# Kernel tuning notes

Hardware: AMD Instinct MI355X
Metric: run time of the kernel (lower is better)

The kernel has to match this reference:

```python
import jax, jax.numpy as jnp
import numpy as np

T = 1048576      # signal length
K = 3            # number of IMFs
ALPHA = 2000.0   # bandwidth penalty
TAU = 1e-7       # dual ascent step
TOL = 1e-6       # convergence tolerance
N_ITER = 50      # max fixed-point iterations


def _vmd(x, omega_init):
    T_ = x.shape[0]
    t = jnp.arange(1, T_ + 1, dtype=jnp.float32) / T_
    freqs = t - 0.5 - 1.0 / T_                           # [T]
    f_hat = jnp.fft.fftshift(jnp.fft.fft(x))             # [T] complex
    u0 = jnp.zeros((K, T_), dtype=f_hat.dtype)
    lam0 = jnp.zeros((T_,), dtype=f_hat.dtype)

    def step(carry, n):
        u_prev, lam_prev, omega, done = carry
        base = (freqs[None, :] - omega[:, None]) ** 2    # [K,T]
        # mode k's denom also gets (freqs-omega[k-1])^2 and (freqs-omega[k+1])^2
        nbr = jnp.zeros_like(base).at[1:].add(base[:-1]).at[:-1].add(base[1:])
        denom = base + nbr + TAU ** 2
        u_hat = (f_hat[None, :] - lam_prev[None, :] / 2.0) / (1.0 + ALPHA * denom)
        pw = jnp.real(u_hat) ** 2 + jnp.imag(u_hat) ** 2  # |u_hat|^2, [K,T]
        omega_new = jnp.sum(freqs[None, :] * pw, axis=1) / jnp.sum(pw, axis=1)
        lam_new = lam_prev + TAU * (jnp.sum(u_hat, axis=0) - f_hat)
        # convergence check (every 10th iter), mirrors the original break
        u_diff = jnp.sum(jnp.abs(u_hat - u_prev) ** 2) / jnp.sum(jnp.abs(u_prev) ** 2)
        om_diff = jnp.sum(jnp.abs(omega_new - jnp.roll(omega_new, 1))) / K
        conv = (n % 10 == 0) & (u_diff < TOL) & (om_diff < TOL)
        # freeze state once converged (break-iteration's fresh u_hat is kept)
        u_out = jnp.where(done, u_prev, u_hat)
        lam_out = jnp.where(done, lam_prev, lam_new)
        om_out = jnp.where(done, omega, omega_new)
        return (u_out, lam_out, om_out, done | conv), None

    init = (u0, lam0, omega_init.astype(jnp.float32), jnp.array(False))
    (u_hat, _, _, _), _ = jax.lax.scan(jax.checkpoint(step), init, jnp.arange(N_ITER))
    imfs = jnp.real(jnp.fft.ifft(jnp.fft.ifftshift(u_hat, axes=-1), axis=-1))
    return imfs.astype(jnp.float32)                      # [K,T]


def setup_inputs() -> dict:
    key = jax.random.key(0)
    kx, ko = jax.random.split(key)
    x = jax.random.normal(kx, (T,), dtype=jnp.float32)
    omega_init = jax.random.uniform(ko, (K,), dtype=jnp.float32) * 0.5  # init==1
    return {"x": x, "omega_init": omega_init}


def reference(x, omega_init):
    return _vmd(x, omega_init)
```

## Files before the change

kernel.cpp:

```cpp
#include <hip/hip_runtime.h>
#include <math.h>


#define ALPHA_F 2000.0f
#define TAU_F   1e-7f

static __device__ __forceinline__ int lpad2(int i) { return i + (i >> 4); }
static __device__ __forceinline__ int swz(int i)  { return ((i & 7) << 7) | (i >> 3); }
static __device__ __forceinline__ int swzA(int i) { return ((i & 7) << 6) | (i >> 3); }
static __device__ __forceinline__ float frcp(float x) { return __builtin_amdgcn_rcpf(x); }

typedef float v2f __attribute__((ext_vector_type(2)));
static __device__ __forceinline__ v2f sp(float s) { v2f r; r.x = s; r.y = s; return r; }
static __device__ __forceinline__ v2f v2(float a, float b) { v2f r; r.x = a; r.y = b; return r; }
static __device__ __forceinline__ v2f pkfma(v2f a, v2f b, v2f c)
{ return __builtin_elementwise_fma(a, b, c); }
static __device__ __forceinline__ v2f cmul(v2f a, v2f w)
{
  v2f t = a * sp(w.x);
  v2f s = v2(-a.y, a.x);
  return pkfma(s, sp(w.y), t);
}
static __device__ __forceinline__ v2f cmulrr(v2f a, float wr, float wi)
{
  v2f t = a * sp(wr);
  v2f s = v2(-a.y, a.x);
  return pkfma(s, sp(wi), t);
}

#define PADN2 1088

template<int CTRL>
static __device__ __forceinline__ float dpp_addf(float v)
{
  int r = __builtin_amdgcn_update_dpp(0, __float_as_int(v), CTRL, 0xf, 0xf, true);
  return v + __int_as_float(r);
}
static __device__ __forceinline__ float wave64_sum(float v)
{
  v = dpp_addf<0x111>(v);
  v = dpp_addf<0x112>(v);
  v = dpp_addf<0x114>(v);
  v = dpp_addf<0x118>(v);
  v = dpp_addf<0x142>(v);
  v = dpp_addf<0x143>(v);
  return v;
}
static __device__ __forceinline__ float row8_sum(float v)
{
  v = dpp_addf<0x111>(v);
  v = dpp_addf<0x112>(v);
  v = dpp_addf<0x114>(v);
  return v;
}
static __device__ __forceinline__ float rdlane(float v, int l)
{
  return __int_as_float(__builtin_amdgcn_readlane(__float_as_int(v), l));
}

template<int SIGN>
static __device__ __forceinline__ void bfly4(v2f Y0, v2f Y1, v2f Y2, v2f Y3,
    float w1r, float w1i, float w2r, float w2i, float w3r, float w3i,
    v2f& o0, v2f& o1, v2f& o2, v2f& o3)
{
  v2f y1 = cmulrr(Y1, w1r, w1i), y2 = cmulrr(Y2, w2r, w2i),
      y3 = cmulrr(Y3, w3r, w3i);
  v2f t0 = Y0 + y2, t1 = Y0 - y2, t2 = y1 + y3, t3 = y1 - y3;
  o0 = t0 + t2; o2 = t0 - t2;
  v2f ns3 = v2(t3.y, -t3.x);
  if (SIGN < 0) { o1 = t1 + ns3; o3 = t1 - ns3; }
  else          { o1 = t1 - ns3; o3 = t1 + ns3; }
}
template<int SIGN>
static __device__ __forceinline__ void bfly4_nt(v2f X0, v2f X1, v2f X2, v2f X3,
    v2f& o0, v2f& o1, v2f& o2, v2f& o3)
{
  v2f t0 = X0 + X2, t1 = X0 - X2, t2 = X1 + X3, t3 = X1 - X3;
  o0 = t0 + t2; o2 = t0 - t2;
  v2f ns3 = v2(t3.y, -t3.x);
  if (SIGN < 0) { o1 = t1 + ns3; o3 = t1 - ns3; }
  else          { o1 = t1 - ns3; o3 = t1 + ns3; }
}

template<int SIGN>
static __device__ void fft1024p_reg(v2f X0, v2f X1, v2f X2, v2f X3,
                                    v2f* A, v2f* B)
{
  const int u = threadIdx.x;
  {
    v2f o0, o1, o2, o3;
    bfly4_nt<SIGN>(X0, X1, X2, X3, o0, o1, o2, o3);
    const int base = u << 2;
    B[lpad2(base    )] = o0; B[lpad2(base + 1)] = o1;
    B[lpad2(base + 2)] = o2; B[lpad2(base + 3)] = o3;
    __syncthreads();
  }
#pragma unroll
  for (int st = 1; st < 5; ++st) {
    v2f *in  = (st & 1) ? B : A;
    v2f *out = (st & 1) ? A : B;
    const int quarter = 1 << (2 * st);
    const int p = u & (quarter - 1);
    const int g = u >> (2 * st);

    float sw, cw;
    sincospif((float)(2 * p) * (1.0f / (float)(4 << (2 * st))), &sw, &cw);
    const float w1r = cw, w1i = (SIGN < 0) ? -sw : sw;
    const float w2r = w1r * w1r - w1i * w1i, w2i = 2.0f * w1r * w1i;
    const float w3r = w2r * w1r - w2i * w1i, w3i = w2r * w1i + w2i * w1r;

    v2f o0, o1, o2, o3;
    bfly4<SIGN>(in[lpad2(u)], in[lpad2(u + 256)],
                in[lpad2(u + 512)], in[lpad2(u + 768)],
                w1r, w1i, w2r, w2i, w3r, w3i, o0, o1, o2, o3);

    const int base = (g << (2 * st + 2)) + p;
    out[lpad2(base              )] = o0;
    out[lpad2(base +     quarter)] = o1;
    out[lpad2(base + 2 * quarter)] = o2;
    out[lpad2(base + 3 * quarter)] = o3;
    __syncthreads();
  }
}

template<int SIGN>
static __device__ void fft1024p_dual(const v2f X[4], const v2f Y[4],
                                     v2f* A1, v2f* B1, v2f* A2, v2f* B2)
{
  const int u = threadIdx.x;
  {
    v2f o0, o1, o2, o3, p0, p1, p2, p3;
    bfly4_nt<SIGN>(X[0], X[1], X[2], X[3], o0, o1, o2, o3);
    bfly4_nt<SIGN>(Y[0], Y[1], Y[2], Y[3], p0, p1, p2, p3);
    const int base = u << 2;
    B1[lpad2(base    )] = o0; B1[lpad2(base + 1)] = o1;
    B1[lpad2(base + 2)] = o2; B1[lpad2(base + 3)] = o3;
    B2[lpad2(base    )] = p0; B2[lpad2(base + 1)] = p1;
    B2[lpad2(base + 2)] = p2; B2[lpad2(base + 3)] = p3;
    __syncthreads();
  }
#pragma unroll
  for (int st = 1; st < 5; ++st) {
    v2f *in1  = (st & 1) ? B1 : A1, *out1 = (st & 1) ? A1 : B1;
    v2f *in2  = (st & 1) ? B2 : A2, *out2 = (st & 1) ? A2 : B2;
    const int quarter = 1 << (2 * st);
    const int p = u & (quarter - 1);
    const int g = u >> (2 * st);

    float sw, cw;
    sincospif((float)(2 * p) * (1.0f / (float)(4 << (2 * st))), &sw, &cw);
    const float w1r = cw, w1i = (SIGN < 0) ? -sw : sw;
    const float w2r = w1r * w1r - w1i * w1i, w2i = 2.0f * w1r * w1i;
    const float w3r = w2r * w1r - w2i * w1i, w3i = w2r * w1i + w2i * w1r;

    v2f o0, o1, o2, o3, p0, p1, p2, p3;
    bfly4<SIGN>(in1[lpad2(u)], in1[lpad2(u + 256)],
                in1[lpad2(u + 512)], in1[lpad2(u + 768)],
                w1r, w1i, w2r, w2i, w3r, w3i, o0, o1, o2, o3);
    bfly4<SIGN>(in2[lpad2(u)], in2[lpad2(u + 256)],
                in2[lpad2(u + 512)], in2[lpad2(u + 768)],
                w1r, w1i, w2r, w2i, w3r, w3i, p0, p1, p2, p3);

    const int base = (g << (2 * st + 2)) + p;
    out1[lpad2(base              )] = o0;
    out1[lpad2(base +     quarter)] = o1;
    out1[lpad2(base + 2 * quarter)] = o2;
    out1[lpad2(base + 3 * quarter)] = o3;
    out2[lpad2(base              )] = p0;
    out2[lpad2(base +     quarter)] = p1;
    out2[lpad2(base + 2 * quarter)] = p2;
    out2[lpad2(base + 3 * quarter)] = p3;
    __syncthreads();
  }
}

__global__ __launch_bounds__(256) void k_fwd_passA(const float* __restrict__ x,
                                                   float2* __restrict__ ws0)
{
  __shared__ __align__(16) v2f A[PADN2], B[PADN2];
  const int p = swzA(blockIdx.x);
  const int tid = threadIdx.x;
  const int c0 = 2 * p;
  v2f X[4];
#pragma unroll
  for (int q = 0; q < 4; ++q)
    X[q] = ((const v2f*)x)[(size_t)(tid + 256 * q) * 512 + p];
  fft1024p_reg<-1>(X[0], X[1], X[2], X[3], A, B);

  float sa, ca, sb, cb, ssa, cca, ssb, ccb;
  sincospif((float)(c0 * tid) * (2.0f / 1048576.0f), &sa, &ca);
  sincospif((float)((c0 + 1) * tid) * (2.0f / 1048576.0f), &sb, &cb);
  sincospif((float)c0 * (1.0f / 2048.0f), &ssa, &cca);
  sincospif((float)(c0 + 1) * (1.0f / 2048.0f), &ssb, &ccb);
  v2f E0 = v2(ca, -sa), E1 = v2(cb, -sb);
  const v2f S0 = v2(cca, -ssa), S1 = v2(ccb, -ssb);
#pragma unroll
  for (int q = 0; q < 4; ++q) {
    int k = tid + 256 * q;
    int kk = (1024 - k) & 1023;
    v2f Z = B[lpad2(k)];
    v2f Wv = B[lpad2(kk)];
    float X0r = 0.5f * (Z.x + Wv.x), X0i = 0.5f * (Z.y - Wv.y);
    float X1r = 0.5f * (Z.y + Wv.y), X1i = 0.5f * (Wv.x - Z.x);
    v2f o01 = cmul(v2(X0r, X0i), E0);
    v2f o23 = cmul(v2(X1r, X1i), E1);
    float4 o = make_float4(o01.x, o01.y, o23.x, o23.y);
    ((float4*)ws0)[(size_t)k * 512 + p] = o;
    E0 = cmul(E0, S0); E1 = cmul(E1, S1);
  }
}

__global__ __launch_bounds__(256) void k_fwd_passB(const float2* __restrict__ ws0,
                                                   float2* __restrict__ fhat,
                                                   float* __restrict__ ET)
{
  __shared__ __align__(16) v2f A[PADN2], B[PADN2];
  const int b = swz(blockIdx.x);
  const int tid = threadIdx.x;
  v2f X[4];
#pragma unroll
  for (int q = 0; q < 4; ++q)
    X[q] = ((const v2f*)ws0)[(size_t)b * 1024 + tid + 256 * q];
  fft1024p_reg<-1>(X[0], X[1], X[2], X[3], A, B);
#pragma unroll
  for (int q = 0; q < 4; ++q) {
    int k2 = tid + 256 * q;
    v2f v = B[lpad2(k2)];
    fhat[(size_t)b * 1024 + k2] = make_float2(v.x, v.y);
    ET[(size_t)k2 * 1024 + b] = v.x * v.x + v.y * v.y;
  }
}

static __device__ __forceinline__ void lag4(float x, float& l0, float& l1,
                                            float& l2, float& l3)
{
  float m0 = x, m1 = x - (1.0f / 3.0f), m2 = x - (2.0f / 3.0f), m3 = x - 1.0f;
  l0 = -4.5f * m1 * m2 * m3;
  l1 = 13.5f * m0 * m2 * m3;
  l2 = -13.5f * m0 * m1 * m3;
  l3 =  4.5f * m0 * m1 * m2;
}

__global__ __launch_bounds__(256) void k_moments(const float* __restrict__ ET,
                                                 double* __restrict__ W)
{
  __shared__ double red[4 * 4];
  const int B = blockIdx.x;
  const int k2 = B ^ 512;
  const int tid = threadIdx.x;
  double a0 = 0, a1 = 0, a2 = 0, a3 = 0;
#pragma unroll
  for (int q = 0; q < 4; ++q) {
    int k1 = tid + 256 * q;
    float e = ET[(size_t)k2 * 1024 + k1];
    float l0, l1, l2, l3;
    lag4((float)k1 * (1.0f / 1024.0f), l0, l1, l2, l3);
    a0 += (double)(e * l0); a1 += (double)(e * l1);
    a2 += (double)(e * l2); a3 += (double)(e * l3);
  }
  const int lane = tid & 63, wv = tid >> 6;
  double pv[4] = { a0, a1, a2, a3 };
#pragma unroll
  for (int j = 0; j < 4; ++j) {
    double v = pv[j];
    for (int off = 32; off; off >>= 1) v += __shfl_down(v, off, 64);
    if (lane == 0) red[wv * 4 + j] = v;
  }
  __syncthreads();
  if (tid < 4)
    W[B * 4 + tid] = red[tid] + red[4 + tid] + red[8 + tid] + red[12 + tid];
}

__global__ __launch_bounds__(512) void k_solve(
    const double* __restrict__ W4, const float* __restrict__ omega_init,
    float* __restrict__ ckeepN, float* __restrict__ omegaF)
{
  __shared__ float red[2][64];
  const int t = threadIdx.x;
  const int lane = t & 63, wv = t >> 6;

  float Wsc[8], fsc[8];
#pragma unroll
  for (int e = 0; e < 8; ++e) {
    Wsc[e] = (float)W4[t * 8 + e];
    int bin = 2 * t + (e >> 2);
    fsc[e] = (float)((double)bin / 1024.0 + (double)(e & 3) / 3072.0 - 0.5);
  }
  v2f frA[4], WrA[4], WfA[4], cnA[4];
#pragma unroll
  for (int i = 0; i < 4; ++i) {
    frA[i] = v2(fsc[2 * i], fsc[2 * i + 1]);
    WrA[i] = v2(Wsc[2 * i], Wsc[2 * i + 1]);
    WfA[i] = WrA[i] * frA[i];
    cnA[i] = sp(0.0f);
  }
  float om0 = omega_init[0], om1 = omega_init[1], om2 = omega_init[2];

#pragma unroll 1
  for (int it = 0; it < 49; ++it) {
    float* rb = red[it & 1];
    v2f p0 = sp(0.f), p1 = sp(0.f), p2 = sp(0.f),
        p3 = sp(0.f), p4 = sp(0.f), p5 = sp(0.f);

#pragma unroll
    for (int i = 0; i < 4; ++i) {
      const v2f fv = frA[i];
      v2f a0 = fv - sp(om0), a1 = fv - sp(om1), a2 = fv - sp(om2);
      v2f d0 = a0 * a0, d1 = a1 * a1, d2 = a2 * a2;
      v2f s01 = d0 + d1, s12 = d1 + d2;
      v2f dA = pkfma(sp(ALPHA_F), s01, sp(1.0f));
      v2f dC = pkfma(sp(ALPHA_F), s12, sp(1.0f));
      v2f dB = pkfma(sp(ALPHA_F), d2, dA);
      v2f AB = dA * dB, BC = dB * dC, AC = dA * dC;
      v2f ABC = AB * dC;
      float rr = frcp(ABC.x * ABC.y);
      v2f r = v2(rr * ABC.y, rr * ABC.x);
      v2f w0 = BC * r, w1 = AC * r, w2 = AB * r;
      v2f hf = pkfma(sp(-0.5f), cnA[i], sp(1.0f));
      v2f g = hf * hf;
      v2f gw0 = g * (w0 * w0), gw1 = g * (w1 * w1), gw2 = g * (w2 * w2);
      p0 = pkfma(WfA[i], gw0, p0); p1 = pkfma(WfA[i], gw1, p1);
      p2 = pkfma(WfA[i], gw2, p2);
      p3 = pkfma(WrA[i], gw0, p3); p4 = pkfma(WrA[i], gw1, p4);
      p5 = pkfma(WrA[i], gw2, p5);
      v2f S = (w0 + w1) + w2;
      cnA[i] = pkfma(sp(TAU_F), pkfma(S, hf, sp(-1.0f)), cnA[i]);
    }

    float q0 = p0.x + p0.y, q1 = p1.x + p1.y, q2 = p2.x + p2.y;
    float q3 = p3.x + p3.y, q4 = p4.x + p4.y, q5 = p5.x + p5.y;

    q0 = wave64_sum(q0); q1 = wave64_sum(q1); q2 = wave64_sum(q2);
    q3 = wave64_sum(q3); q4 = wave64_sum(q4); q5 = wave64_sum(q5);
    if (lane == 63) {
      rb[0 * 8 + wv] = q0; rb[1 * 8 + wv] = q1; rb[2 * 8 + wv] = q2;
      rb[3 * 8 + wv] = q3; rb[4 * 8 + wv] = q4; rb[5 * 8 + wv] = q5;
    }
    __syncthreads();
    float v1 = rb[lane];
    v1 = row8_sum(v1);
    float n0 = rdlane(v1, 7),  n1 = rdlane(v1, 15), n2 = rdlane(v1, 23);
    float e0 = rdlane(v1, 31), e1 = rdlane(v1, 39), e2 = rdlane(v1, 47);
    om0 = n0 * frcp(e0);
    om1 = n1 * frcp(e1);
    om2 = n2 * frcp(e2);
  }

  ((float4*)ckeepN)[2 * t]     = make_float4(cnA[0].x, cnA[0].y, cnA[1].x, cnA[1].y);
  ((float4*)ckeepN)[2 * t + 1] = make_float4(cnA[2].x, cnA[2].y, cnA[3].x, cnA[3].y);
  if (t == 0) { omegaF[0] = om0; omegaF[1] = om1; omegaF[2] = om2; }
}

__global__ __launch_bounds__(256) void k_inv_A2(
    const float2* __restrict__ fhat, const float* __restrict__ ckeepN,
    const float* __restrict__ omegaF, float2* __restrict__ ws0)
{
  __shared__ __align__(16) v2f A1[PADN2], B1[PADN2], A2[PADN2], B2[PADN2];
  const int tid = threadIdx.x;
  const int b = swz(blockIdx.x);
  const float om0 = omegaF[0], om1 = omegaF[1], om2 = omegaF[2];
  const float xb = (float)b * (1.0f / 1024.0f);
  float l0, l1, l2, l3, m0, m1, m2, m3;
  lag4(xb, l0, l1, l2, l3);
  lag4(1.0f - xb, m0, m1, m2, m3);
  const float4* cN = (const float4*)ckeepN;

  v2f X[4];
  v2f Y[4];
#pragma unroll
  for (int q = 0; q < 4; ++q) {
    int j = tid + 256 * q;
    float2 f = fhat[(size_t)b * 1024 + j];
    int bin = j ^ 512;
    int binp = 1023 - bin;
    float4 cv = cN[bin];
    float4 cw = cN[binp];
    float c  = l0 * cv.x + l1 * cv.y + l2 * cv.z + l3 * cv.w;
    float cp = m0 * cw.x + m1 * cw.y + m2 * cw.z + m3 * cw.w;
    float hf = 1.0f - 0.5f * c;
    float hp = 1.0f - 0.5f * cp;
    int tt = (bin << 10) | b;
    float freq = (float)tt * (1.0f / 1048576.0f) - 0.5f;
    v2f fpm = v2(freq, -freq);
    v2f A0 = fpm - sp(om0), A1v = fpm - sp(om1), A2v = fpm - sp(om2);
    v2f D0 = A0 * A0, D1 = A1v * A1v, D2 = A2v * A2v;
    v2f DA = pkfma(sp(ALPHA_F), D0 + D1, sp(1.0f));
    v2f DB = pkfma(sp(ALPHA_F), D2, DA);
    float r0 = hf * frcp(DA.x), r0n = hp * frcp(DA.y);
    float r1 = hf * frcp(DB.x), r1n = hp * frcp(DB.y);
    float Rr = 0.5f * (r0 + r0n), Ri = 0.5f * (r1 + r1n);
    X[q] = cmul(v2(f.x, f.y), v2(Rr, Ri));
    v2f DC = pkfma(sp(ALPHA_F), D1 + D2, sp(1.0f));
    float r2 = hf * frcp(DC.x), r2n = hp * frcp(DC.y);
    float Rr2 = 0.5f * (r2 + r2n);
    Y[q] = v2(f.x, f.y) * sp(Rr2);
  }
  fft1024p_dual<1>(X, Y, A1, B1, A2, B2);

  float sa, ca, ss, cs;
  sincospif((float)(b * tid) * (2.0f / 1048576.0f), &sa, &ca);
  sincospif((float)b * (1.0f / 2048.0f), &ss, &cs);
  v2f E = v2(ca, sa);
  const v2f S = v2(cs, ss);
#pragma unroll
  for (int q = 0; q < 4; ++q) {
    int m1i = tid + 256 * q;
    v2f va = B1[lpad2(m1i)];
    v2f vb = B2[lpad2(m1i)];
    v2f oa = cmul(va, E);
    v2f ob = cmul(vb, E);
    ws0[(size_t)m1i * 1024 + b]           = make_float2(oa.x, oa.y);
    ws0[1048576 + (size_t)m1i * 1024 + b] = make_float2(ob.x, ob.y);
    E = cmul(E, S);
  }
}

__global__ __launch_bounds__(256) void k_inv_B2(const float2* __restrict__ ws0,
                                                float* __restrict__ out)
{
  __shared__ __align__(16) v2f A[PADN2], B[PADN2];
  const int tid = threadIdx.x;
  const float sc = 1.0f / 1048576.0f;

  if (blockIdx.x < 1024) {
    const int b = swz(blockIdx.x);
    v2f X[4];
#pragma unroll
    for (int q = 0; q < 4; ++q)
      X[q] = ((const v2f*)ws0)[(size_t)b * 1024 + tid + 256 * q];
    fft1024p_reg<1>(X[0], X[1], X[2], X[3], A, B);
#pragma unroll
    for (int q = 0; q < 4; ++q) {
      int m2 = tid + 256 * q;
      v2f v = B[lpad2(m2)];
      out[(size_t)m2 * 1024 + b]           = v.x * sc;
      out[1048576 + (size_t)m2 * 1024 + b] = v.y * sc;
    }
  } else {
    const int s = swzA(blockIdx.x - 1024);
    const int b0 = 2 * s, b1 = 2 * s + 1;
#pragma unroll
    for (int q = 0; q < 4; ++q) {
      int j = tid + 256 * q;
      A[lpad2(j)] = ((const v2f*)ws0)[1048576 + (size_t)b0 * 1024 + j];
      B[lpad2(j)] = ((const v2f*)ws0)[1048576 + (size_t)b1 * 1024 + j];
    }
    __syncthreads();
    v2f Z[4];
#pragma unroll
    for (int q = 0; q < 4; ++q) {
      int j = tid + 256 * q;
      int mj = (1024 - j) & 1023;
      v2f W0j = A[lpad2(j)], W0m = A[lpad2(mj)];
      v2f W1j = B[lpad2(j)], W1m = B[lpad2(mj)];
      float H0r = 0.5f * (W0j.x + W0m.x), H0i = 0.5f * (W0j.y - W0m.y);
      float H1r = 0.5f * (W1j.x + W1m.x), H1i = 0.5f * (W1j.y - W1m.y);
      Z[q] = v2(H0r - H1i, H0i + H1r);
    }
    __syncthreads();
    fft1024p_reg<1>(Z[0], Z[1], Z[2], Z[3], A, B);
#pragma unroll
    for (int q = 0; q < 4; ++q) {
      int m2 = tid + 256 * q;
      v2f v = B[lpad2(m2)];
      out[2097152 + (size_t)m2 * 1024 + b0] = v.x * sc;
      out[2097152 + (size_t)m2 * 1024 + b1] = v.y * sc;
    }
  }
}

extern "C" void kernel_launch(void* const* d_in, const int* in_sizes, int n_in,
                              void* d_out, int out_size, void* d_ws, size_t ws_size,
                              hipStream_t stream)
{
  (void)in_sizes; (void)n_in; (void)out_size; (void)ws_size;
  const float* x       = (const float*)d_in[0];
  const float* om_init = (const float*)d_in[1];
  float* out = (float*)d_out;

  char* w = (char*)d_ws;
  const size_t MB = 1024ull * 1024ull;
  float2* fhat     = (float2*)(w);
  float*  ET       = (float*)(w + 8 * MB);
  double* W4       = (double*)(w + 12 * MB);
  float*  ckeepN   = (float*)(w + 12 * MB + 32 * 1024);
  float*  omegaF   = (float*)(w + 12 * MB + 48 * 1024);
  float2* scratch  = (float2*)(w + 16 * MB);

  k_fwd_passA<<<512, 256, 0, stream>>>(x, scratch);
  k_fwd_passB<<<1024, 256, 0, stream>>>(scratch, fhat, ET);
  k_moments<<<1024, 256, 0, stream>>>(ET, W4);
  k_solve<<<1, 512, 0, stream>>>(W4, om_init, ckeepN, omegaF);
  k_inv_A2<<<1024, 256, 0, stream>>>(fhat, ckeepN, omegaF, scratch);
  k_inv_B2<<<1536, 256, 0, stream>>>(scratch, out);
}
```

Before: 170.3 us.

## Exploit Hermitian symmetry of real-input FFT to halve forward and inverse column FFTs

The forward spectrum of the real signal is conjugate-symmetric, so only 513 of the 1024 column FFTs in the second forward pass are computed. Each one also writes its mirrored conjugate into fhat and ET. In the inverse first pass, the second mode's output (real-valued filter on a Hermitian spectrum) is likewise symmetric, so blocks above 512 run a single FFT instead of the dual one, and the lower blocks write the mirrored conjugate column. This removes roughly half of the FFT work at the cost of scattered mirror writes and divergence between blocks.

After: 172.7 us. Within noise of the previous version (+1.4%).

```diff
diff --git a/kernel.cpp b/kernel.cpp
--- a/kernel.cpp
+++ b/kernel.cpp
@@ -204,8 +204,10 @@
     float X1r = 0.5f * (Z.y + Wv.y), X1i = 0.5f * (Wv.x - Z.x);
     v2f o01 = cmul(v2(X0r, X0i), E0);
     v2f o23 = cmul(v2(X1r, X1i), E1);
-    float4 o = make_float4(o01.x, o01.y, o23.x, o23.y);
-    ((float4*)ws0)[(size_t)k * 512 + p] = o;
+    if (k <= 512) {
+      float4 o = make_float4(o01.x, o01.y, o23.x, o23.y);
+      ((float4*)ws0)[(size_t)k * 512 + p] = o;
+    }
     E0 = cmul(E0, S0); E1 = cmul(E1, S1);
   }
 }
@@ -215,19 +217,25 @@
                                                    float* __restrict__ ET)
 {
   __shared__ __align__(16) v2f A[PADN2], B[PADN2];
-  const int b = swz(blockIdx.x);
+  const int b = blockIdx.x;
   const int tid = threadIdx.x;
   v2f X[4];
 #pragma unroll
   for (int q = 0; q < 4; ++q)
     X[q] = ((const v2f*)ws0)[(size_t)b * 1024 + tid + 256 * q];
   fft1024p_reg<-1>(X[0], X[1], X[2], X[3], A, B);
+  const bool mir = (b >= 1) && (b <= 511);
 #pragma unroll
   for (int q = 0; q < 4; ++q) {
     int k2 = tid + 256 * q;
     v2f v = B[lpad2(k2)];
+    float e = v.x * v.x + v.y * v.y;
     fhat[(size_t)b * 1024 + k2] = make_float2(v.x, v.y);
-    ET[(size_t)k2 * 1024 + b] = v.x * v.x + v.y * v.y;
+    ET[(size_t)k2 * 1024 + b] = e;
+    if (mir) {
+      fhat[(size_t)(1024 - b) * 1024 + (1023 - k2)] = make_float2(v.x, -v.y);
+      ET[(size_t)(1023 - k2) * 1024 + (1024 - b)] = e;
+    }
   }
 }
 
@@ -358,6 +366,7 @@
   __shared__ __align__(16) v2f A1[PADN2], B1[PADN2], A2[PADN2], B2[PADN2];
   const int tid = threadIdx.x;
   const int b = swz(blockIdx.x);
+  const bool dual = (b <= 512);
   const float om0 = omegaF[0], om1 = omegaF[1], om2 = omegaF[2];
   const float xb = (float)b * (1.0f / 1024.0f);
   float l0, l1, l2, l3, m0, m1, m2, m3;
@@ -390,28 +399,46 @@
     float r1 = hf * frcp(DB.x), r1n = hp * frcp(DB.y);
     float Rr = 0.5f * (r0 + r0n), Ri = 0.5f * (r1 + r1n);
     X[q] = cmul(v2(f.x, f.y), v2(Rr, Ri));
-    v2f DC = pkfma(sp(ALPHA_F), D1 + D2, sp(1.0f));
-    float r2 = hf * frcp(DC.x), r2n = hp * frcp(DC.y);
-    float Rr2 = 0.5f * (r2 + r2n);
-    Y[q] = v2(f.x, f.y) * sp(Rr2);
-  }
-  fft1024p_dual<1>(X, Y, A1, B1, A2, B2);
+    if (dual) {
+      v2f DC = pkfma(sp(ALPHA_F), D1 + D2, sp(1.0f));
+      float r2 = hf * frcp(DC.x), r2n = hp * frcp(DC.y);
+      float Rr2 = 0.5f * (r2 + r2n);
+      Y[q] = v2(f.x, f.y) * sp(Rr2);
+    }
+  }
 
   float sa, ca, ss, cs;
   sincospif((float)(b * tid) * (2.0f / 1048576.0f), &sa, &ca);
   sincospif((float)b * (1.0f / 2048.0f), &ss, &cs);
   v2f E = v2(ca, sa);
   const v2f S = v2(cs, ss);
-#pragma unroll
-  for (int q = 0; q < 4; ++q) {
-    int m1i = tid + 256 * q;
-    v2f va = B1[lpad2(m1i)];
-    v2f vb = B2[lpad2(m1i)];
-    v2f oa = cmul(va, E);
-    v2f ob = cmul(vb, E);
-    ws0[(size_t)m1i * 1024 + b]           = make_float2(oa.x, oa.y);
-    ws0[1048576 + (size_t)m1i * 1024 + b] = make_float2(ob.x, ob.y);
-    E = cmul(E, S);
+
+  if (dual) {
+    fft1024p_dual<1>(X, Y, A1, B1, A2, B2);
+    const bool mir = (b >= 1) && (b <= 511);
+#pragma unroll
+    for (int q = 0; q < 4; ++q) {
+      int m1i = tid + 256 * q;
+      v2f va = B1[lpad2(m1i)];
+      v2f vb = B2[lpad2(m1i)];
+      v2f oa = cmul(va, E);
+      v2f ob = cmul(vb, E);
+      ws0[(size_t)m1i * 1024 + b]           = make_float2(oa.x, oa.y);
+      ws0[1048576 + (size_t)m1i * 1024 + b] = make_float2(ob.x, ob.y);
+      if (mir)
+        ws0[1048576 + (size_t)m1i * 1024 + (1024 - b)] = make_float2(ob.x, -ob.y);
+      E = cmul(E, S);
+    }
+  } else {
+    fft1024p_reg<1>(X[0], X[1], X[2], X[3], A1, B1);
+#pragma unroll
+    for (int q = 0; q < 4; ++q) {
+      int m1i = tid + 256 * q;
+      v2f va = B1[lpad2(m1i)];
+      v2f oa = cmul(va, E);
+      ws0[(size_t)m1i * 1024 + b] = make_float2(oa.x, oa.y);
+      E = cmul(E, S);
+    }
   }
 }
 
@@ -488,7 +515,7 @@
   float2* scratch  = (float2*)(w + 16 * MB);
 
   k_fwd_passA<<<512, 256, 0, stream>>>(x, scratch);
-  k_fwd_passB<<<1024, 256, 0, stream>>>(scratch, fhat, ET);
+  k_fwd_passB<<<513, 256, 0, stream>>>(scratch, fhat, ET);
   k_moments<<<1024, 256, 0, stream>>>(ET, W4);
   k_solve<<<1, 512, 0, stream>>>(W4, om_init, ckeepN, omegaF);
   k_inv_A2<<<1024, 256, 0, stream>>>(fhat, ckeepN, omegaF, scratch);
```
